# Optimization experiments

Measured on AMD Instinct MI355X. Metric: run time of the kernel, lower is better.

Reference implementation:

```python
import jax, jax.numpy as jnp
import numpy as np

N = 100000   # nodes
E = 1600000  # edges
D = 64       # in_channel == out_channel
NEG_SLOPE = 0.01  # nn.LeakyReLU default


def gcn_conv(x, W, b, src, dst, n):
    # PyG GCNConv: add self-loops, sym-normalize by in-degree (at col/dst),
    # norm(e) = deg[src]^-1/2 * deg[dst]^-1/2, aggregate at dst, then + bias.
    deg = jnp.zeros((n,), x.dtype).at[dst].add(1.0) + 1.0  # in-degree incl. self-loop
    dinv = jax.lax.rsqrt(deg)
    h = x @ W                                   # [N, Dout]
    coef = (dinv[src] * dinv[dst])[:, None]     # [E, 1]
    agg = jax.ops.segment_sum(h[src] * coef, dst, num_segments=n)  # scatter-add
    # self-loop contribution: deg[i]^-1 * h[i]
    return agg + (dinv * dinv)[:, None] * h + b


def setup_inputs() -> dict:
    key = jax.random.key(0)
    ks = jax.random.split(key, 10)
    x = jax.random.normal(ks[0], (N, D), dtype=jnp.float32)
    edge_index = jax.random.randint(ks[1], (2, E), 0, N)
    s = 1.0 / np.sqrt(D)  # glorot-ish scale
    inp = {"x": x, "edge_index": edge_index}
    for i in range(4):
        inp[f"W{i+1}"] = jax.random.normal(ks[2 + i], (D, D), dtype=jnp.float32) * s
        inp[f"b{i+1}"] = jnp.zeros((D,), dtype=jnp.float32)
    return inp


def reference(x, edge_index, W1, b1, W2, b2, W3, b3, W4, b4):
    # eval mode: F.dropout(training=False) is identity, so omitted.
    src, dst = edge_index[0], edge_index[1]
    h = x
    for W, b in ((W1, b1), (W2, b2), (W3, b3), (W4, b4)):
        h = gcn_conv(h, W, b, src, dst, N)
        h = jnp.where(h >= 0, h, NEG_SLOPE * h)  # LeakyReLU
    return h
```

## Files before the change

### kernel.cpp

```cpp
#include <hip/hip_runtime.h>
#include <hip/hip_fp16.h>

#define N_NODES 100000
#define N_EDGES 1600000
#define DIM 64
#define NEG_SLOPE 0.01f

#define BNODES 64
#define NBUCK 1563
#define BCAP 2048
#define BLOCKS1 256
#define THREADS1 512
#define EPB (N_EDGES / BLOCKS1)

typedef _Float16 half8 __attribute__((ext_vector_type(8)));
typedef float float4v __attribute__((ext_vector_type(4)));

__global__ void prep_weights(const float* __restrict__ W0, const float* __restrict__ W1,
                             const float* __restrict__ W2, const float* __restrict__ W3,
                             __half* __restrict__ WT16, int* __restrict__ gcur) {
    if (blockIdx.x < 4) {
        const float* Ws[4] = {W0, W1, W2, W3};
        const float* W = Ws[blockIdx.x];
        __half* dst = WT16 + (size_t)blockIdx.x * DIM * DIM;
        for (int e = threadIdx.x; e < DIM * DIM; e += 256) {
            int k = e >> 6, f = e & 63;
            dst[f * DIM + k] = __float2half(W[e]);
        }
    } else {
        for (int i = (blockIdx.x - 4) * 256 + threadIdx.x; i < NBUCK * 16; i += 4 * 256)
            gcur[i] = 0;
    }
}

__global__ __launch_bounds__(THREADS1) void bucket_scatter(const int* __restrict__ src,
                                                           const int* __restrict__ dst,
                                                           int* __restrict__ gcur,
                                                           int* __restrict__ bdata) {
    __shared__ int cnt[NBUCK];
    __shared__ int base[NBUCK];

    const int tid = threadIdx.x;
    for (int i = tid; i < NBUCK; i += THREADS1) cnt[i] = 0;
    __syncthreads();

    const int e0 = blockIdx.x * EPB;
    const int e1 = e0 + EPB;

    for (int e = e0 + tid; e < e1; e += THREADS1)
        atomicAdd(&cnt[dst[e] >> 6], 1);
    __syncthreads();

    for (int i = tid; i < NBUCK; i += THREADS1) {
        int c = cnt[i];
        base[i] = c ? atomicAdd(&gcur[i * 16], c) : 0;
        cnt[i] = 0;
    }
    __syncthreads();

    for (int e = e0 + tid; e < e1; e += THREADS1) {
        int d = dst[e];
        int b = d >> 6;
        int p = atomicAdd(&cnt[b], 1);
        bdata[(size_t)b * BCAP + base[b] + p] = src[e] | ((d & 63) << 17);
    }
}

__global__ __launch_bounds__(256) void bucket_build(const int* __restrict__ bdata,
                                                    const int* __restrict__ gcur,
                                                    int* __restrict__ offsets,
                                                    float* __restrict__ dinv,
                                                    int* __restrict__ csr) {
    __shared__ int cnt[BNODES];
    __shared__ int excl[BNODES];
    __shared__ int part[256];
    const int tid = threadIdx.x;
    const int b = blockIdx.x;
    const int sz = gcur[b * 16];
    const int* bd = bdata + (size_t)b * BCAP;

    int s = 0;
    for (int i = tid; i < b; i += 256) s += gcur[i * 16];
    part[tid] = s;
    __syncthreads();
    for (int st = 128; st > 0; st >>= 1) {
        if (tid < st) part[tid] += part[tid + st];
        __syncthreads();
    }
    const int cbase = part[0];
    __syncthreads();

    for (int i = tid; i < BNODES; i += 256) cnt[i] = 0;
    __syncthreads();
    for (int i = tid; i < sz; i += 256)
        atomicAdd(&cnt[bd[i] >> 17], 1);
    __syncthreads();
    if (tid == 0) {
        int run = 0;
        for (int j = 0; j < BNODES; ++j) { excl[j] = run; run += cnt[j]; }
    }
    __syncthreads();

    const int nb = b * BNODES;
    for (int i = tid; i < BNODES; i += 256) {
        int n = nb + i;
        if (n < N_NODES) {
            offsets[n] = cbase + excl[i];
            dinv[n] = rsqrtf((float)(cnt[i] + 1));
        }
    }
    if (b == NBUCK - 1 && tid == 0) offsets[N_NODES] = N_EDGES;

    for (int i = tid; i < BNODES; i += 256) cnt[i] = 0;
    __syncthreads();
    for (int i = tid; i < sz; i += 256) {
        int v = bd[i];
        int l = v >> 17;
        int pos = cbase + excl[l] + atomicAdd(&cnt[l], 1);
        csr[pos] = (v & 0x1FFFF) << 6;
    }
}

__device__ __forceinline__ void stage8(__half* dst, const float* __restrict__ X, size_t off) {
    float4 f0 = *(const float4*)(X + off);
    float4 f1 = *(const float4*)(X + off + 4);
    __half2 h0 = __floats2half2_rn(f0.x, f0.y);
    __half2 h1 = __floats2half2_rn(f0.z, f0.w);
    __half2 h2 = __floats2half2_rn(f1.x, f1.y);
    __half2 h3 = __floats2half2_rn(f1.z, f1.w);
    uint4 u;
    u.x = *(unsigned int*)&h0; u.y = *(unsigned int*)&h1;
    u.z = *(unsigned int*)&h2; u.w = *(unsigned int*)&h3;
    *(uint4*)dst = u;
}
__device__ __forceinline__ void stage8(__half* dst, const __half* __restrict__ X, size_t off) {
    *(uint4*)dst = *(const uint4*)(X + off);
}

#define XPAD 72
template <typename TIN>
__global__ __launch_bounds__(256) void mm_kernel(const TIN* __restrict__ X,
                                                 const __half* __restrict__ WT,
                                                 const float* __restrict__ dinv,
                                                 __half* __restrict__ G16) {
    __shared__ __align__(16) __half xs[64][XPAD];
    __shared__ __align__(16) __half ws[64][XPAD];
    const int t = threadIdx.x;
    const int rbase = blockIdx.x * 64;

    for (int c = t; c < 512; c += 256) {
        int row = c >> 3, koff = (c & 7) * 8;
        int grow = rbase + row;
        if (grow < N_NODES) {
            stage8(&xs[row][koff], X, (size_t)grow * DIM + koff);
        } else {
            *(uint4*)&xs[row][koff] = make_uint4(0, 0, 0, 0);
        }
        stage8(&ws[row][koff], WT, (size_t)row * DIM + koff);
    }
    __syncthreads();

    const int wave = t >> 6;
    const int lane = t & 63;
    const int q = lane >> 4;
    const int c16 = lane & 15;
    const int n0 = wave * 16;

    half8 b0 = *(const half8*)&xs[n0 + c16][q * 8];
    half8 b1 = *(const half8*)&xs[n0 + c16][32 + q * 8];

    const int gnode = rbase + n0 + c16;
    float di = (gnode < N_NODES) ? dinv[gnode] : 0.f;

#pragma unroll
    for (int ft = 0; ft < 4; ++ft) {
        const int f0 = ft * 16;
        half8 a0 = *(const half8*)&ws[f0 + c16][q * 8];
        half8 a1 = *(const half8*)&ws[f0 + c16][32 + q * 8];
        float4v acc = {0.f, 0.f, 0.f, 0.f};
        acc = __builtin_amdgcn_mfma_f32_16x16x32_f16(a0, b0, acc, 0, 0, 0);
        acc = __builtin_amdgcn_mfma_f32_16x16x32_f16(a1, b1, acc, 0, 0, 0);
        if (gnode < N_NODES) {
            __half2 p0 = __floats2half2_rn(di * acc[0], di * acc[1]);
            __half2 p1 = __floats2half2_rn(di * acc[2], di * acc[3]);
            uint2 u;
            u.x = *(unsigned int*)&p0;
            u.y = *(unsigned int*)&p1;
            *(uint2*)(G16 + (size_t)gnode * DIM + f0 + q * 4) = u;
        }
    }
}

__global__ __launch_bounds__(256) void fused_agg_mm(const __half* __restrict__ Gin,
                                                    const int* __restrict__ csr,
                                                    const int* __restrict__ offsets,
                                                    const float* __restrict__ dinv,
                                                    const float* __restrict__ bias,
                                                    const __half* __restrict__ WT,
                                                    __half* __restrict__ Gout) {
    __shared__ __align__(16) __half act[64][XPAD];
    __shared__ __align__(16) __half ws[64][XPAD];
    const int t = threadIdx.x;
    const int blk = blockIdx.x;
    const int nb = blk * BNODES;

    for (int c = t; c < 512; c += 256) {
        int row = c >> 3, koff = (c & 7) * 8;
        stage8(&ws[row][koff], WT, (size_t)row * DIM + koff);
    }

    const int wave = t >> 6;
    const int lane = t & 63;
    const int grp  = lane >> 5;
    const int slot = (lane >> 3) & 3;
    const int sub  = lane & 7;
    const int fc   = sub * 8;

    for (int i = 0; i < 8; ++i) {
        const int lrow = wave * 16 + i * 2 + grp;
        const int wid = nb + lrow;
        const bool valid = (wid < N_NODES);
        const int beg = valid ? offsets[wid] : 0;
        const int end = valid ? offsets[wid + 1] : 0;

        __half2 h0 = __float2half2_rn(0.f), h1 = h0, h2 = h0, h3 = h0;

#define PKACC(vraw)                                     \
        {                                               \
            const __half2* hp = (const __half2*)&(vraw);\
            h0 = __hadd2(h0, hp[0]);                    \
            h1 = __hadd2(h1, hp[1]);                    \
            h2 = __hadd2(h2, hp[2]);                    \
            h3 = __hadd2(h3, hp[3]);                    \
        }
        int e = beg + slot;
        for (; e + 4 < end; e += 8) {
            int p0 = csr[e];
            int p1 = csr[e + 4];
            float4 v0 = *(const float4*)(Gin + (size_t)p0 + fc);
            float4 v1 = *(const float4*)(Gin + (size_t)p1 + fc);
            PKACC(v0)
            PKACC(v1)
        }
        if (e < end) {
            int p0 = csr[e];
            float4 v0 = *(const float4*)(Gin + (size_t)p0 + fc);
            PKACC(v0)
        }
#undef PKACC

        float acc[8];
        {
            float2 f;
            f = __half22float2(h0); acc[0] = f.x; acc[1] = f.y;
            f = __half22float2(h1); acc[2] = f.x; acc[3] = f.y;
            f = __half22float2(h2); acc[4] = f.x; acc[5] = f.y;
            f = __half22float2(h3); acc[6] = f.x; acc[7] = f.y;
        }
#pragma unroll
        for (int k = 0; k < 8; ++k) {
            acc[k] += __shfl_xor(acc[k], 8, 64);
            acc[k] += __shfl_xor(acc[k], 16, 64);
        }

        if (slot == 0) {
            uint4 u = make_uint4(0, 0, 0, 0);
            if (valid) {
                float4 vs = *(const float4*)(Gin + (size_t)wid * DIM + fc);
                {
                    const __half2* hp = (const __half2*)&vs;
                    float2 f0 = __half22float2(hp[0]);
                    float2 f1 = __half22float2(hp[1]);
                    float2 f2 = __half22float2(hp[2]);
                    float2 f3 = __half22float2(hp[3]);
                    acc[0] += f0.x; acc[1] += f0.y;
                    acc[2] += f1.x; acc[3] += f1.y;
                    acc[4] += f2.x; acc[5] += f2.y;
                    acc[6] += f3.x; acc[7] += f3.y;
                }
                float di = dinv[wid];
                float4 bb0 = *(const float4*)(bias + fc);
                float4 bb1 = *(const float4*)(bias + fc + 4);
                float r[8];
                r[0] = di * acc[0] + bb0.x;
                r[1] = di * acc[1] + bb0.y;
                r[2] = di * acc[2] + bb0.z;
                r[3] = di * acc[3] + bb0.w;
                r[4] = di * acc[4] + bb1.x;
                r[5] = di * acc[5] + bb1.y;
                r[6] = di * acc[6] + bb1.z;
                r[7] = di * acc[7] + bb1.w;
#pragma unroll
                for (int k = 0; k < 8; ++k)
                    r[k] = (r[k] >= 0.f) ? r[k] : NEG_SLOPE * r[k];
                __half2 q0 = __floats2half2_rn(r[0], r[1]);
                __half2 q1 = __floats2half2_rn(r[2], r[3]);
                __half2 q2 = __floats2half2_rn(r[4], r[5]);
                __half2 q3 = __floats2half2_rn(r[6], r[7]);
                u.x = *(unsigned int*)&q0;
                u.y = *(unsigned int*)&q1;
                u.z = *(unsigned int*)&q2;
                u.w = *(unsigned int*)&q3;
            }
            *(uint4*)(&act[lrow][fc]) = u;
        }
    }
    __syncthreads();

    const int q = lane >> 4;
    const int c16 = lane & 15;
    const int n0 = wave * 16;

    half8 xb0 = *(const half8*)&act[n0 + c16][q * 8];
    half8 xb1 = *(const half8*)&act[n0 + c16][32 + q * 8];

    const int gnode = nb + n0 + c16;
    float dio = (gnode < N_NODES) ? dinv[gnode] : 0.f;

#pragma unroll
    for (int ft = 0; ft < 4; ++ft) {
        const int f0 = ft * 16;
        half8 a0 = *(const half8*)&ws[f0 + c16][q * 8];
        half8 a1 = *(const half8*)&ws[f0 + c16][32 + q * 8];
        float4v accv = {0.f, 0.f, 0.f, 0.f};
        accv = __builtin_amdgcn_mfma_f32_16x16x32_f16(a0, xb0, accv, 0, 0, 0);
        accv = __builtin_amdgcn_mfma_f32_16x16x32_f16(a1, xb1, accv, 0, 0, 0);
        if (gnode < N_NODES) {
            __half2 p0 = __floats2half2_rn(dio * accv[0], dio * accv[1]);
            __half2 p1 = __floats2half2_rn(dio * accv[2], dio * accv[3]);
            uint2 u;
            u.x = *(unsigned int*)&p0;
            u.y = *(unsigned int*)&p1;
            *(uint2*)(Gout + (size_t)gnode * DIM + f0 + q * 4) = u;
        }
    }
}

#define AGG_BLOCKS 2048
#define AGG_WAVES (AGG_BLOCKS * 4)
#define NPAIRS (N_NODES / 2)
template <bool FINAL>
__global__ __launch_bounds__(256) void agg_kernel(const __half* __restrict__ G16,
                                                  const int* __restrict__ csr,
                                                  const int* __restrict__ offsets,
                                                  const float* __restrict__ dinv,
                                                  const float* __restrict__ bias,
                                                  void* __restrict__ outp) {
    const int gw = (blockIdx.x * 256 + threadIdx.x) >> 6;
    const int lane = threadIdx.x & 63;
    const int grp  = lane >> 5;
    const int slot = (lane >> 3) & 3;
    const int sub  = lane & 7;
    const int fc   = sub * 8;

    for (int p = gw; p < NPAIRS; p += AGG_WAVES) {
        const int wid = p * 2 + grp;
        const int beg = offsets[wid], end = offsets[wid + 1];

        __half2 h0 = __float2half2_rn(0.f), h1 = h0, h2 = h0, h3 = h0;

#define PKACC(vraw)                                     \
        {                                               \
            const __half2* hp = (const __half2*)&(vraw);\
            h0 = __hadd2(h0, hp[0]);                    \
            h1 = __hadd2(h1, hp[1]);                    \
            h2 = __hadd2(h2, hp[2]);                    \
            h3 = __hadd2(h3, hp[3]);                    \
        }

        int e = beg + slot;
        for (; e + 4 < end; e += 8) {
            int p0 = csr[e];
            int p1 = csr[e + 4];
            float4 v0 = *(const float4*)(G16 + (size_t)p0 + fc);
            float4 v1 = *(const float4*)(G16 + (size_t)p1 + fc);
            PKACC(v0)
            PKACC(v1)
        }
        if (e < end) {
            int p0 = csr[e];
            float4 v0 = *(const float4*)(G16 + (size_t)p0 + fc);
            PKACC(v0)
        }
#undef PKACC

        float acc[8];
        {
            float2 f;
            f = __half22float2(h0); acc[0] = f.x; acc[1] = f.y;
            f = __half22float2(h1); acc[2] = f.x; acc[3] = f.y;
            f = __half22float2(h2); acc[4] = f.x; acc[5] = f.y;
            f = __half22float2(h3); acc[6] = f.x; acc[7] = f.y;
        }
#pragma unroll
        for (int k = 0; k < 8; ++k) {
            acc[k] += __shfl_xor(acc[k], 8, 64);
            acc[k] += __shfl_xor(acc[k], 16, 64);
        }

        if (slot == 0) {
            float4 vs = *(const float4*)(G16 + (size_t)wid * DIM + fc);
            {
                const __half2* hp = (const __half2*)&vs;
                float2 f0 = __half22float2(hp[0]);
                float2 f1 = __half22float2(hp[1]);
                float2 f2 = __half22float2(hp[2]);
                float2 f3 = __half22float2(hp[3]);
                acc[0] += f0.x; acc[1] += f0.y;
                acc[2] += f1.x; acc[3] += f1.y;
                acc[4] += f2.x; acc[5] += f2.y;
                acc[6] += f3.x; acc[7] += f3.y;
            }

            float di = dinv[wid];
            float4 b0 = *(const float4*)(bias + fc);
            float4 b1 = *(const float4*)(bias + fc + 4);
            float r[8];
            r[0] = di * acc[0] + b0.x;
            r[1] = di * acc[1] + b0.y;
            r[2] = di * acc[2] + b0.z;
            r[3] = di * acc[3] + b0.w;
            r[4] = di * acc[4] + b1.x;
            r[5] = di * acc[5] + b1.y;
            r[6] = di * acc[6] + b1.z;
            r[7] = di * acc[7] + b1.w;
#pragma unroll
            for (int k = 0; k < 8; ++k)
                r[k] = (r[k] >= 0.f) ? r[k] : NEG_SLOPE * r[k];

            if (FINAL) {
                float* out = (float*)outp;
                *(float4*)(out + (size_t)wid * DIM + fc)     = make_float4(r[0], r[1], r[2], r[3]);
                *(float4*)(out + (size_t)wid * DIM + fc + 4) = make_float4(r[4], r[5], r[6], r[7]);
            } else {
                __half* act = (__half*)outp;
                __half2 q0 = __floats2half2_rn(r[0], r[1]);
                __half2 q1 = __floats2half2_rn(r[2], r[3]);
                __half2 q2 = __floats2half2_rn(r[4], r[5]);
                __half2 q3 = __floats2half2_rn(r[6], r[7]);
                uint4 u;
                u.x = *(unsigned int*)&q0;
                u.y = *(unsigned int*)&q1;
                u.z = *(unsigned int*)&q2;
                u.w = *(unsigned int*)&q3;
                *(uint4*)(act + (size_t)wid * DIM + fc) = u;
            }
        }
    }
}

extern "C" void kernel_launch(void* const* d_in, const int* in_sizes, int n_in,
                              void* d_out, int out_size, void* d_ws, size_t ws_size,
                              hipStream_t stream) {
    const float* x = (const float*)d_in[0];
    const int* ei = (const int*)d_in[1];
    const int* src = ei;
    const int* dst = ei + N_EDGES;
    const float* W[4] = {(const float*)d_in[2], (const float*)d_in[4],
                         (const float*)d_in[6], (const float*)d_in[8]};
    const float* b[4] = {(const float*)d_in[3], (const float*)d_in[5],
                         (const float*)d_in[7], (const float*)d_in[9]};
    float* out = (float*)d_out;

    char* ws = (char*)d_ws;
    size_t off = 0;
    auto alloc = [&](size_t bytes) -> void* {
        void* p = ws + off;
        off = (off + bytes + 255) & ~(size_t)255;
        return p;
    };
    __half* GA    = (__half*)alloc((size_t)N_NODES * DIM * sizeof(__half));
    __half* GB    = (__half*)alloc((size_t)N_NODES * DIM * sizeof(__half));
    __half* WT16  = (__half*)alloc((size_t)4 * DIM * DIM * sizeof(__half));
    int*   csr    = (int*)alloc((size_t)N_EDGES * sizeof(int));
    int*   bdata  = (int*)alloc((size_t)NBUCK * BCAP * sizeof(int));
    int*   gcur   = (int*)alloc((size_t)NBUCK * 16 * sizeof(int));
    int*   offsets= (int*)alloc((size_t)(N_NODES + 1) * sizeof(int));
    float* dinv   = (float*)alloc((size_t)N_NODES * sizeof(float));

    prep_weights<<<8, 256, 0, stream>>>(W[0], W[1], W[2], W[3], WT16, gcur);

    bucket_scatter<<<BLOCKS1, THREADS1, 0, stream>>>(src, dst, gcur, bdata);
    bucket_build<<<NBUCK, 256, 0, stream>>>(bdata, gcur, offsets, dinv, csr);

    const int MM_GRID = (N_NODES + 63) / 64;

    mm_kernel<float><<<MM_GRID, 256, 0, stream>>>(x, WT16, dinv, GA);
    fused_agg_mm<<<NBUCK, 256, 0, stream>>>(GA, csr, offsets, dinv, b[0], WT16 + 1 * DIM * DIM, GB);
    fused_agg_mm<<<NBUCK, 256, 0, stream>>>(GB, csr, offsets, dinv, b[1], WT16 + 2 * DIM * DIM, GA);
    fused_agg_mm<<<NBUCK, 256, 0, stream>>>(GA, csr, offsets, dinv, b[2], WT16 + 3 * DIM * DIM, GB);
    agg_kernel<true><<<AGG_BLOCKS, 256, 0, stream>>>(GB, csr, offsets, dinv, b[3], out);
}
```

Measured before the change: 294.5 us.

## Coarsen CSR build buckets and locally sort edges before coalesced bucket writes

The CSR preprocessing now uses 256-node buckets (391 of them) instead of 64-node buckets, and each scatter block sorts its edge slice in LDS by bucket before writing. The sorted slice is written out as contiguous runs per bucket, replacing scattered single-int global stores. Scatter blocks double to 512, and bucket_build runs fewer, larger blocks. The risks are more LDS use per scatter block, higher bucket capacity that could overflow under skewed degree distributions, and less parallelism in the build stage.

```diff
diff --git a/kernel.cpp b/kernel.cpp
--- a/kernel.cpp
+++ b/kernel.cpp
@@ -6,12 +6,15 @@
 #define DIM 64
 #define NEG_SLOPE 0.01f
 
-#define BNODES 64
-#define NBUCK 1563
-#define BCAP 2048
-#define BLOCKS1 256
+#define PNODES 256
+#define PNB 391
+#define BCAP 4608
+#define BLOCKS1 512
 #define THREADS1 512
 #define EPB (N_EDGES / BLOCKS1)
+
+#define FNODES 64
+#define FNB 1563
 
 typedef _Float16 half8 __attribute__((ext_vector_type(8)));
 typedef float float4v __attribute__((ext_vector_type(4)));
@@ -28,7 +31,7 @@
             dst[f * DIM + k] = __float2half(W[e]);
         }
     } else {
-        for (int i = (blockIdx.x - 4) * 256 + threadIdx.x; i < NBUCK * 16; i += 4 * 256)
+        for (int i = (blockIdx.x - 4) * 256 + threadIdx.x; i < PNB * 16; i += 4 * 256)
             gcur[i] = 0;
     }
 }
@@ -37,21 +40,38 @@
                                                            const int* __restrict__ dst,
                                                            int* __restrict__ gcur,
                                                            int* __restrict__ bdata) {
-    __shared__ int cnt[NBUCK];
-    __shared__ int base[NBUCK];
+    __shared__ int cnt[PNB];
+    __shared__ int lexcl[PNB];
+    __shared__ int base[PNB];
+    __shared__ int wsum[THREADS1 / 64];
+    __shared__ int sorted_e[EPB];
+    __shared__ unsigned short sorted_b[EPB];
 
     const int tid = threadIdx.x;
-    for (int i = tid; i < NBUCK; i += THREADS1) cnt[i] = 0;
+    for (int i = tid; i < PNB; i += THREADS1) cnt[i] = 0;
     __syncthreads();
 
     const int e0 = blockIdx.x * EPB;
     const int e1 = e0 + EPB;
 
     for (int e = e0 + tid; e < e1; e += THREADS1)
-        atomicAdd(&cnt[dst[e] >> 6], 1);
-    __syncthreads();
-
-    for (int i = tid; i < NBUCK; i += THREADS1) {
+        atomicAdd(&cnt[dst[e] >> 8], 1);
+    __syncthreads();
+
+    int v = (tid < PNB) ? cnt[tid] : 0;
+    int incl = v;
+#pragma unroll
+    for (int s = 1; s < 64; s <<= 1) {
+        int up = __shfl_up(incl, s, 64);
+        if ((tid & 63) >= s) incl += up;
+    }
+    if ((tid & 63) == 63) wsum[tid >> 6] = incl;
+    __syncthreads();
+    int wpre = 0;
+    for (int w = 0; w < (tid >> 6); ++w) wpre += wsum[w];
+    if (tid < PNB) lexcl[tid] = wpre + incl - v;
+
+    for (int i = tid; i < PNB; i += THREADS1) {
         int c = cnt[i];
         base[i] = c ? atomicAdd(&gcur[i * 16], c) : 0;
         cnt[i] = 0;
@@ -60,9 +80,16 @@
 
     for (int e = e0 + tid; e < e1; e += THREADS1) {
         int d = dst[e];
-        int b = d >> 6;
-        int p = atomicAdd(&cnt[b], 1);
-        bdata[(size_t)b * BCAP + base[b] + p] = src[e] | ((d & 63) << 17);
+        int b = d >> 8;
+        int p = lexcl[b] + atomicAdd(&cnt[b], 1);
+        sorted_e[p] = src[e] | ((d & 255) << 17);
+        sorted_b[p] = (unsigned short)b;
+    }
+    __syncthreads();
+
+    for (int i = tid; i < EPB; i += THREADS1) {
+        int b = sorted_b[i];
+        bdata[(size_t)b * BCAP + base[b] + (i - lexcl[b])] = sorted_e[i];
     }
 }
 
@@ -71,8 +98,8 @@
                                                     int* __restrict__ offsets,
                                                     float* __restrict__ dinv,
                                                     int* __restrict__ csr) {
-    __shared__ int cnt[BNODES];
-    __shared__ int excl[BNODES];
+    __shared__ int cnt[PNODES];
+    __shared__ int excl[PNODES];
     __shared__ int part[256];
     const int tid = threadIdx.x;
     const int b = blockIdx.x;
@@ -90,28 +117,28 @@
     const int cbase = part[0];
     __syncthreads();
 
-    for (int i = tid; i < BNODES; i += 256) cnt[i] = 0;
+    for (int i = tid; i < PNODES; i += 256) cnt[i] = 0;
     __syncthreads();
     for (int i = tid; i < sz; i += 256)
         atomicAdd(&cnt[bd[i] >> 17], 1);
     __syncthreads();
     if (tid == 0) {
         int run = 0;
-        for (int j = 0; j < BNODES; ++j) { excl[j] = run; run += cnt[j]; }
-    }
-    __syncthreads();
-
-    const int nb = b * BNODES;
-    for (int i = tid; i < BNODES; i += 256) {
+        for (int j = 0; j < PNODES; ++j) { excl[j] = run; run += cnt[j]; }
+    }
+    __syncthreads();
+
+    const int nb = b * PNODES;
+    for (int i = tid; i < PNODES; i += 256) {
         int n = nb + i;
         if (n < N_NODES) {
             offsets[n] = cbase + excl[i];
             dinv[n] = rsqrtf((float)(cnt[i] + 1));
         }
     }
-    if (b == NBUCK - 1 && tid == 0) offsets[N_NODES] = N_EDGES;
-
-    for (int i = tid; i < BNODES; i += 256) cnt[i] = 0;
+    if (b == PNB - 1 && tid == 0) offsets[N_NODES] = N_EDGES;
+
+    for (int i = tid; i < PNODES; i += 256) cnt[i] = 0;
     __syncthreads();
     for (int i = tid; i < sz; i += 256) {
         int v = bd[i];
@@ -202,7 +229,7 @@
     __shared__ __align__(16) __half ws[64][XPAD];
     const int t = threadIdx.x;
     const int blk = blockIdx.x;
-    const int nb = blk * BNODES;
+    const int nb = blk * FNODES;
 
     for (int c = t; c < 512; c += 256) {
         int row = c >> 3, koff = (c & 7) * 8;
@@ -473,21 +500,21 @@
     __half* GB    = (__half*)alloc((size_t)N_NODES * DIM * sizeof(__half));
     __half* WT16  = (__half*)alloc((size_t)4 * DIM * DIM * sizeof(__half));
     int*   csr    = (int*)alloc((size_t)N_EDGES * sizeof(int));
-    int*   bdata  = (int*)alloc((size_t)NBUCK * BCAP * sizeof(int));
-    int*   gcur   = (int*)alloc((size_t)NBUCK * 16 * sizeof(int));
+    int*   bdata  = (int*)alloc((size_t)PNB * BCAP * sizeof(int));
+    int*   gcur   = (int*)alloc((size_t)PNB * 16 * sizeof(int));
     int*   offsets= (int*)alloc((size_t)(N_NODES + 1) * sizeof(int));
     float* dinv   = (float*)alloc((size_t)N_NODES * sizeof(float));
 
     prep_weights<<<8, 256, 0, stream>>>(W[0], W[1], W[2], W[3], WT16, gcur);
 
     bucket_scatter<<<BLOCKS1, THREADS1, 0, stream>>>(src, dst, gcur, bdata);
-    bucket_build<<<NBUCK, 256, 0, stream>>>(bdata, gcur, offsets, dinv, csr);
+    bucket_build<<<PNB, 256, 0, stream>>>(bdata, gcur, offsets, dinv, csr);
 
     const int MM_GRID = (N_NODES + 63) / 64;
 
     mm_kernel<float><<<MM_GRID, 256, 0, stream>>>(x, WT16, dinv, GA);
-    fused_agg_mm<<<NBUCK, 256, 0, stream>>>(GA, csr, offsets, dinv, b[0], WT16 + 1 * DIM * DIM, GB);
-    fused_agg_mm<<<NBUCK, 256, 0, stream>>>(GB, csr, offsets, dinv, b[1], WT16 + 2 * DIM * DIM, GA);
-    fused_agg_mm<<<NBUCK, 256, 0, stream>>>(GA, csr, offsets, dinv, b[2], WT16 + 3 * DIM * DIM, GB);
+    fused_agg_mm<<<FNB, 256, 0, stream>>>(GA, csr, offsets, dinv, b[0], WT16 + 1 * DIM * DIM, GB);
+    fused_agg_mm<<<FNB, 256, 0, stream>>>(GB, csr, offsets, dinv, b[1], WT16 + 2 * DIM * DIM, GA);
+    fused_agg_mm<<<FNB, 256, 0, stream>>>(GA, csr, offsets, dinv, b[2], WT16 + 3 * DIM * DIM, GB);
     agg_kernel<true><<<AGG_BLOCKS, 256, 0, stream>>>(GB, csr, offsets, dinv, b[3], out);
 }
```

Result: faster. 287.8 us (-2.3%).
